# Kernel tuning notes

Measured on AMD Instinct MI355X. Metric: run time of the kernel, lower is better.

## Reference

```python
import jax, jax.numpy as jnp
import numpy as np

N_NODES = 100000
IN_DIM = 128
HID = 128
N_EDGES = 1600000
N_PAIRS = 500000


def setup_inputs() -> dict:
    key = jax.random.key(0)
    ks = jax.random.split(key, 16)

    def lin(k, fan_out, fan_in):
        s = 1.0 / np.sqrt(fan_in)
        kw, kb = jax.random.split(k)
        W = jax.random.uniform(kw, (fan_out, fan_in), jnp.float32, -s, s)
        b = jax.random.uniform(kb, (fan_out,), jnp.float32, -s, s)
        return W, b

    x = jax.random.normal(ks[0], (N_NODES, IN_DIM), jnp.float32)
    edge_index = jax.random.randint(ks[1], (2, N_EDGES), 0, N_NODES, jnp.int64)
    edge_pairs = jax.random.randint(ks[2], (N_PAIRS, 2), 0, N_NODES, jnp.int64)

    # SAGEConv 1: lin_l (neighbor aggr, with bias), lin_r (root, no bias)
    W1l, b1l = lin(ks[3], HID, IN_DIM)
    W1r, _ = lin(ks[4], HID, IN_DIM)
    # SAGEConv 2
    W2l, b2l = lin(ks[5], HID, HID)
    W2r, _ = lin(ks[6], HID, HID)
    # MLP decoder
    Wm1, bm1 = lin(ks[7], HID, HID)
    Wm2, bm2 = lin(ks[8], HID // 2, HID)
    Wm3, bm3 = lin(ks[9], 1, HID // 2)

    return dict(x=x, edge_index=edge_index, edge_pairs=edge_pairs,
                W1l=W1l, b1l=b1l, W1r=W1r,
                W2l=W2l, b2l=b2l, W2r=W2r,
                Wm1=Wm1, bm1=bm1, Wm2=Wm2, bm2=bm2, Wm3=Wm3, bm3=bm3)


def _sage_conv(x, src, dst, Wl, bl, Wr):
    # mean aggregation of source-node features into destination nodes
    msg_sum = jax.ops.segment_sum(x[src], dst, num_segments=N_NODES)  # [N, D]
    cnt = jax.ops.segment_sum(jnp.ones((src.shape[0],), x.dtype), dst,
                              num_segments=N_NODES)
    aggr = msg_sum / jnp.maximum(cnt, 1.0)[:, None]
    return aggr @ Wl.T + bl + x @ Wr.T


def reference(x, edge_index, edge_pairs,
              W1l, b1l, W1r, W2l, b2l, W2r,
              Wm1, bm1, Wm2, bm2, Wm3, bm3):
    src, dst = edge_index[0], edge_index[1]
    # encode (eval mode: dropout = identity)
    h = jax.nn.relu(_sage_conv(x, src, dst, W1l, b1l, W1r))
    z = _sage_conv(h, src, dst, W2l, b2l, W2r)  # [N, HID]
    # decode
    hp = z[edge_pairs[:, 0]] * z[edge_pairs[:, 1]]  # [P, HID]
    hp = jax.nn.relu(hp @ Wm1.T + bm1)
    hp = jax.nn.relu(hp @ Wm2.T + bm2)
    return (hp @ Wm3.T + bm3).squeeze(-1)  # [P]
```

## Files before the change

kernel.cpp:

```cpp
#include <hip/hip_runtime.h>
#include <stdint.h>

typedef _Float16 half8 __attribute__((ext_vector_type(8)));
typedef float float4v __attribute__((ext_vector_type(4)));

constexpr int kN = 100000;
constexpr int kE = 1600000;
constexpr int kP = 500000;
constexpr int NBS = (kN + 255) / 256;
constexpr int CT2 = kN / 32;
constexpr int DT2 = kP / 32;

__global__ void deg_kernel(const int* __restrict__ dst, int* __restrict__ deg) {
    int e = blockIdx.x * blockDim.x + threadIdx.x;
    if (e < kE) atomicAdd(&deg[dst[e]], 1);
}

__global__ void scan_block_sums(const int* __restrict__ deg, int* __restrict__ bsum) {
    __shared__ int red[256];
    int t = threadIdx.x;
    int i = blockIdx.x * 256 + t;
    red[t] = (i < kN) ? deg[i] : 0;
    __syncthreads();
    for (int s = 128; s > 0; s >>= 1) {
        if (t < s) red[t] += red[t + s];
        __syncthreads();
    }
    if (t == 0) bsum[blockIdx.x] = red[0];
}

__global__ void scan_bsums(const int* __restrict__ bsum, int* __restrict__ boff) {
    __shared__ int sm[512];
    int t = threadIdx.x;
    int orig = (t < NBS) ? bsum[t] : 0;
    sm[t] = orig;
    __syncthreads();
    for (int d = 1; d < 512; d <<= 1) {
        int u = (t >= d) ? sm[t - d] : 0;
        __syncthreads();
        sm[t] += u;
        __syncthreads();
    }
    if (t < NBS) boff[t] = sm[t] - orig;
}

__global__ void scan_write(const int* __restrict__ deg, const int* __restrict__ boff,
                           int* __restrict__ row_start, int* __restrict__ cursor) {
    __shared__ int sm[256];
    int t = threadIdx.x;
    int i = blockIdx.x * 256 + t;
    int v = (i < kN) ? deg[i] : 0;
    sm[t] = v;
    __syncthreads();
    for (int d = 1; d < 256; d <<= 1) {
        int u = (t >= d) ? sm[t - d] : 0;
        __syncthreads();
        sm[t] += u;
        __syncthreads();
    }
    int excl = sm[t] - v + boff[blockIdx.x];
    if (i < kN) { row_start[i] = excl; cursor[i] = excl; }
    if (i == kN - 1) row_start[kN] = excl + v;
}

__global__ void fill_kernel(const int* __restrict__ src, const int* __restrict__ dst,
                            int* __restrict__ cursor, int* __restrict__ srcs) {
    int e = blockIdx.x * blockDim.x + threadIdx.x;
    if (e < kE) {
        int p = atomicAdd(&cursor[dst[e]], 1);
        srcs[p] = src[e];
    }
}

__global__ void cvt_x_kernel(const float* __restrict__ x, _Float16* __restrict__ xh) {
    const int i = (blockIdx.x * 256 + threadIdx.x) * 8;
    if (i >= kN * 128) return;
    const float4 a = *(const float4*)&x[i];
    const float4 b = *(const float4*)&x[i + 4];
    half8 v;
    v[0] = (_Float16)a.x; v[1] = (_Float16)a.y; v[2] = (_Float16)a.z; v[3] = (_Float16)a.w;
    v[4] = (_Float16)b.x; v[5] = (_Float16)b.y; v[6] = (_Float16)b.z; v[7] = (_Float16)b.w;
    *(half8*)&xh[i] = v;
}

__global__ void cvt_w_kernel(
    const float* __restrict__ W1l, const float* __restrict__ W1r,
    const float* __restrict__ W2l, const float* __restrict__ W2r,
    const float* __restrict__ Wm1, const float* __restrict__ Wm2,
    _Float16* __restrict__ CW1h, _Float16* __restrict__ CW1e,
    _Float16* __restrict__ CW2h, _Float16* __restrict__ CW2e,
    _Float16* __restrict__ M1h,  _Float16* __restrict__ M2h)
{
    const int i = blockIdx.x * 256 + threadIdx.x;
    if (i < 32768) {
        const int o = i >> 8, k = i & 255;
        const float w = (k < 128) ? W1l[o * 128 + k] : W1r[o * 128 + k - 128];
        const _Float16 h = (_Float16)w;
        CW1h[i] = h; CW1e[i] = (_Float16)(w - (float)h);
    } else if (i < 65536) {
        const int j = i - 32768;
        const int o = j >> 8, k = j & 255;
        const float w = (k < 128) ? W2l[o * 128 + k] : W2r[o * 128 + k - 128];
        const _Float16 h = (_Float16)w;
        CW2h[j] = h; CW2e[j] = (_Float16)(w - (float)h);
    } else if (i < 81920) {
        const int j = i - 65536;
        M1h[j] = (_Float16)Wm1[j];
    } else if (i < 90112) {
        const int j = i - 81920;
        M2h[j] = (_Float16)Wm2[j];
    }
}

template <bool RELU>
__global__ __launch_bounds__(256, 3) void conv_mfma(
    const _Float16* __restrict__ xin,
    const int* __restrict__ row_start,
    const int* __restrict__ srcs,
    const _Float16* __restrict__ Wh,
    const _Float16* __restrict__ We,
    const float* __restrict__ bias,
    _Float16* __restrict__ out)
{
    __shared__ __align__(16) _Float16 stg_all[4 * 32 * 136];
    const int wInB = threadIdx.x >> 6;
    _Float16* stg  = &stg_all[wInB * (32 * 136)];
    const int l = threadIdx.x & 63;
    const int p = l & 15;
    const int q = l >> 4;
    const int tile = blockIdx.x * 4 + wInB;
    if (tile >= CT2) return;
    const int c = p * 8;
    const int lbase = l & 48;

    for (int sub = 0; sub < 8; sub++) {
        const int n  = tile * 32 + sub * 4 + q;
        const int j0 = row_start[n], j1 = row_start[n + 1];
        const int cnt = j1 - j0;
        float facc[8];
#pragma unroll
        for (int u = 0; u < 8; u++) facc[u] = 0.f;

        for (int jc = j0; jc < j1; jc += 16) {
            const int m = j1 - jc;
            const int myidx = (jc + p < j1) ? srcs[jc + p] : 0;
            half8 rows[16];
#pragma unroll
            for (int i = 0; i < 16; i++) {
                const int s = __shfl(myidx, lbase + i);
                rows[i] = *(const half8*)&xin[(size_t)s * 128 + c];
            }
#pragma unroll
            for (int i = 0; i < 16; i++) {
                if (i < m) {
#pragma unroll
                    for (int u = 0; u < 8; u++) facc[u] += (float)rows[i][u];
                }
            }
        }
        const float inv = 1.0f / (float)(cnt > 1 ? cnt : 1);
        half8 hv;
#pragma unroll
        for (int u = 0; u < 8; u++) hv[u] = (_Float16)(facc[u] * inv);
        *(half8*)&stg[(sub * 4 + q) * 136 + c] = hv;
    }

    half8 rt[2][4];
#pragma unroll
    for (int m = 0; m < 2; m++)
#pragma unroll
        for (int kt = 0; kt < 4; kt++)
            rt[m][kt] = *(const half8*)&xin[(size_t)(tile * 32 + m * 16 + p) * 128 + kt * 32 + q * 8];

    half8 amf[2][4];
#pragma unroll
    for (int m = 0; m < 2; m++)
#pragma unroll
        for (int kt = 0; kt < 4; kt++)
            amf[m][kt] = *(const half8*)&stg[(m * 16 + p) * 136 + kt * 32 + q * 8];

    float4v acc[2][8];
#pragma unroll
    for (int nt = 0; nt < 8; nt++) {
        const float b = bias[nt * 16 + p];
#pragma unroll
        for (int m = 0; m < 2; m++) {
            acc[m][nt][0] = b; acc[m][nt][1] = b; acc[m][nt][2] = b; acc[m][nt][3] = b;
        }
    }
#pragma unroll
    for (int kt = 0; kt < 8; kt++) {
        const half8 a0 = (kt < 4) ? amf[0][kt] : rt[0][kt - 4];
        const half8 a1 = (kt < 4) ? amf[1][kt] : rt[1][kt - 4];
#pragma unroll
        for (int nt = 0; nt < 8; nt++) {
            const int widx = (nt * 16 + p) * 256 + kt * 32 + q * 8;
            const half8 bh = *(const half8*)&Wh[widx];
            const half8 be = *(const half8*)&We[widx];
            acc[0][nt] = __builtin_amdgcn_mfma_f32_16x16x32_f16(a0, bh, acc[0][nt], 0, 0, 0);
            acc[0][nt] = __builtin_amdgcn_mfma_f32_16x16x32_f16(a0, be, acc[0][nt], 0, 0, 0);
            acc[1][nt] = __builtin_amdgcn_mfma_f32_16x16x32_f16(a1, bh, acc[1][nt], 0, 0, 0);
            acc[1][nt] = __builtin_amdgcn_mfma_f32_16x16x32_f16(a1, be, acc[1][nt], 0, 0, 0);
        }
    }

#pragma unroll
    for (int m = 0; m < 2; m++)
#pragma unroll
        for (int nt = 0; nt < 8; nt++)
#pragma unroll
            for (int r = 0; r < 4; r++) {
                float v = acc[m][nt][r];
                if (RELU) v = fmaxf(v, 0.f);
                stg[(m * 16 + q * 4 + r) * 136 + nt * 16 + p] = (_Float16)v;
            }
#pragma unroll
    for (int it = 0; it < 8; it++) {
        const int row = it * 4 + q;
        *(half8*)&out[(size_t)(tile * 32 + row) * 128 + c] =
            *(const half8*)&stg[row * 136 + c];
    }
}

__global__ __launch_bounds__(256, 3) void decoder_mfma(
    const _Float16* __restrict__ z,
    const int* __restrict__ pairs,
    const _Float16* __restrict__ M1h, const float* __restrict__ bm1,
    const _Float16* __restrict__ M2h, const float* __restrict__ bm2,
    const float* __restrict__ Wm3, const float* __restrict__ bm3,
    float* __restrict__ outv)
{
    __shared__ __align__(16) _Float16 buf_all[4 * 32 * 136];
    const int wInB = threadIdx.x >> 6;
    _Float16* buf  = &buf_all[wInB * (32 * 136)];
    const int l = threadIdx.x & 63;
    const int p = l & 15;
    const int q = l >> 4;
    const int tile = blockIdx.x * 4 + wInB;
    if (tile >= DT2) return;
    const int c = p * 8;

    int2 ab[8];
#pragma unroll
    for (int it = 0; it < 8; it++)
        ab[it] = *(const int2*)&pairs[(size_t)(tile * 32 + it * 4 + q) * 2];
    half8 za[8], zb[8];
#pragma unroll
    for (int it = 0; it < 8; it++) {
        za[it] = *(const half8*)&z[(size_t)ab[it].x * 128 + c];
        zb[it] = *(const half8*)&z[(size_t)ab[it].y * 128 + c];
    }
#pragma unroll
    for (int it = 0; it < 8; it++)
        *(half8*)&buf[(it * 4 + q) * 136 + c] = za[it] * zb[it];

    half8 a1[2][4];
#pragma unroll
    for (int m = 0; m < 2; m++)
#pragma unroll
        for (int kt = 0; kt < 4; kt++)
            a1[m][kt] = *(const half8*)&buf[(m * 16 + p) * 136 + kt * 32 + q * 8];

    float4v acc1[2][8];
#pragma unroll
    for (int nt = 0; nt < 8; nt++) {
        const float b = bm1[nt * 16 + p];
#pragma unroll
        for (int m = 0; m < 2; m++) {
            acc1[m][nt][0] = b; acc1[m][nt][1] = b; acc1[m][nt][2] = b; acc1[m][nt][3] = b;
        }
    }
#pragma unroll
    for (int kt = 0; kt < 4; kt++)
#pragma unroll
        for (int nt = 0; nt < 8; nt++) {
            const half8 bh = *(const half8*)&M1h[(nt * 16 + p) * 128 + kt * 32 + q * 8];
            acc1[0][nt] = __builtin_amdgcn_mfma_f32_16x16x32_f16(a1[0][kt], bh, acc1[0][nt], 0, 0, 0);
            acc1[1][nt] = __builtin_amdgcn_mfma_f32_16x16x32_f16(a1[1][kt], bh, acc1[1][nt], 0, 0, 0);
        }

#pragma unroll
    for (int m = 0; m < 2; m++)
#pragma unroll
        for (int nt = 0; nt < 8; nt++)
#pragma unroll
            for (int r = 0; r < 4; r++)
                buf[(m * 16 + q * 4 + r) * 136 + nt * 16 + p] =
                    (_Float16)fmaxf(acc1[m][nt][r], 0.f);

    half8 a2[2][4];
#pragma unroll
    for (int m = 0; m < 2; m++)
#pragma unroll
        for (int kt = 0; kt < 4; kt++)
            a2[m][kt] = *(const half8*)&buf[(m * 16 + p) * 136 + kt * 32 + q * 8];

    float4v acc2[2][4];
#pragma unroll
    for (int nt = 0; nt < 4; nt++) {
        const float b = bm2[nt * 16 + p];
#pragma unroll
        for (int m = 0; m < 2; m++) {
            acc2[m][nt][0] = b; acc2[m][nt][1] = b; acc2[m][nt][2] = b; acc2[m][nt][3] = b;
        }
    }
#pragma unroll
    for (int kt = 0; kt < 4; kt++)
#pragma unroll
        for (int nt = 0; nt < 4; nt++) {
            const half8 bh = *(const half8*)&M2h[(nt * 16 + p) * 128 + kt * 32 + q * 8];
            acc2[0][nt] = __builtin_amdgcn_mfma_f32_16x16x32_f16(a2[0][kt], bh, acc2[0][nt], 0, 0, 0);
            acc2[1][nt] = __builtin_amdgcn_mfma_f32_16x16x32_f16(a2[1][kt], bh, acc2[1][nt], 0, 0, 0);
        }

    float wm3v[4];
#pragma unroll
    for (int nt = 0; nt < 4; nt++) wm3v[nt] = Wm3[nt * 16 + p];
    const float b3 = bm3[0];
#pragma unroll
    for (int m = 0; m < 2; m++) {
        float part[4];
#pragma unroll
        for (int r = 0; r < 4; r++) part[r] = 0.f;
#pragma unroll
        for (int nt = 0; nt < 4; nt++)
#pragma unroll
            for (int r = 0; r < 4; r++)
                part[r] += fmaxf(acc2[m][nt][r], 0.f) * wm3v[nt];
#pragma unroll
        for (int s = 1; s <= 8; s <<= 1)
#pragma unroll
            for (int r = 0; r < 4; r++) part[r] += __shfl_xor(part[r], s);
        if (p == 0) {
            float4 o = make_float4(part[0] + b3, part[1] + b3, part[2] + b3, part[3] + b3);
            *(float4*)&outv[tile * 32 + m * 16 + q * 4] = o;
        }
    }
}

extern "C" void kernel_launch(void* const* d_in, const int* in_sizes, int n_in,
                              void* d_out, int out_size, void* d_ws, size_t ws_size,
                              hipStream_t stream) {
    const float* x   = (const float*)d_in[0];
    const int*   src = (const int*)d_in[1];
    const int*   dst = src + kE;
    const int*   ep  = (const int*)d_in[2];
    const float* W1l = (const float*)d_in[3];
    const float* b1l = (const float*)d_in[4];
    const float* W1r = (const float*)d_in[5];
    const float* W2l = (const float*)d_in[6];
    const float* b2l = (const float*)d_in[7];
    const float* W2r = (const float*)d_in[8];
    const float* Wm1 = (const float*)d_in[9];
    const float* bm1 = (const float*)d_in[10];
    const float* Wm2 = (const float*)d_in[11];
    const float* bm2 = (const float*)d_in[12];
    const float* Wm3 = (const float*)d_in[13];
    const float* bm3 = (const float*)d_in[14];
    float* outv = (float*)d_out;

    char* ws = (char*)d_ws;
    size_t off = 0;
    auto alloc = [&](size_t bytes) -> void* {
        void* p = ws + off;
        off += bytes;
        off = (off + 255) & ~(size_t)255;
        return p;
    };
    int*      deg       = (int*)alloc((size_t)kN * 4);
    int*      row_start = (int*)alloc((size_t)(kN + 1) * 4);
    int*      cursor    = (int*)alloc((size_t)kN * 4);
    int*      bsum      = (int*)alloc(512 * 4);
    int*      boff      = (int*)alloc(512 * 4);
    int*      srcs      = (int*)alloc((size_t)kE * 4);
    _Float16* xh        = (_Float16*)alloc((size_t)kN * 128 * 2);
    _Float16* hh        = (_Float16*)alloc((size_t)kN * 128 * 2);
    _Float16* zh        = (_Float16*)alloc((size_t)kN * 128 * 2);
    _Float16* CW1h      = (_Float16*)alloc(128 * 256 * 2);
    _Float16* CW1e      = (_Float16*)alloc(128 * 256 * 2);
    _Float16* CW2h      = (_Float16*)alloc(128 * 256 * 2);
    _Float16* CW2e      = (_Float16*)alloc(128 * 256 * 2);
    _Float16* M1h       = (_Float16*)alloc(128 * 128 * 2);
    _Float16* M2h       = (_Float16*)alloc(64 * 128 * 2);

    hipMemsetAsync(deg, 0, (size_t)kN * sizeof(int), stream);
    deg_kernel<<<(kE + 255) / 256, 256, 0, stream>>>(dst, deg);
    scan_block_sums<<<NBS, 256, 0, stream>>>(deg, bsum);
    scan_bsums<<<1, 512, 0, stream>>>(bsum, boff);
    scan_write<<<NBS, 256, 0, stream>>>(deg, boff, row_start, cursor);
    fill_kernel<<<(kE + 255) / 256, 256, 0, stream>>>(src, dst, cursor, srcs);

    cvt_x_kernel<<<(kN * 128 / 8 + 255) / 256, 256, 0, stream>>>(x, xh);
    cvt_w_kernel<<<352, 256, 0, stream>>>(W1l, W1r, W2l, W2r, Wm1, Wm2,
                                          CW1h, CW1e, CW2h, CW2e, M1h, M2h);

    const int convBlocks = (CT2 + 3) / 4;
    conv_mfma<true><<<convBlocks, 256, 0, stream>>>(xh, row_start, srcs, CW1h, CW1e, b1l, hh);
    conv_mfma<false><<<convBlocks, 256, 0, stream>>>(hh, row_start, srcs, CW2h, CW2e, b2l, zh);

    const int decBlocks = (DT2 + 3) / 4;
    decoder_mfma<<<decBlocks, 256, 0, stream>>>(
        zh, ep, M1h, bm1, M2h, bm2, Wm3, bm3, outv);
}
```

Before: 686.0 us.

## Software-pipeline neighbor gathers in conv and persistent prefetching decoder

The conv kernel now handles 16-node tiles per wave instead of 32 and raises the occupancy hint. Neighbor-row gathers are double-buffered across four sub-rows, with the first 24 neighbors loaded in 8-row batches and the remainder in a tail loop. The decoder becomes a persistent grid-stride kernel with a fixed grid, prefetching the next tile's pair indices and z rows while the current tile's MLP runs on MFMA. Both changes aim to hide gather latency, at the cost of more register pressure and more complex control flow; the srcs buffer is padded so the speculative index reads stay in bounds.

```diff
diff --git a/kernel.cpp b/kernel.cpp
--- a/kernel.cpp
+++ b/kernel.cpp
@@ -8,7 +8,7 @@
 constexpr int kE = 1600000;
 constexpr int kP = 500000;
 constexpr int NBS = (kN + 255) / 256;
-constexpr int CT2 = kN / 32;
+constexpr int CT3 = kN / 16;
 constexpr int DT2 = kP / 32;
 
 __global__ void deg_kernel(const int* __restrict__ dst, int* __restrict__ deg) {
@@ -113,7 +113,7 @@
 }
 
 template <bool RELU>
-__global__ __launch_bounds__(256, 3) void conv_mfma(
+__global__ __launch_bounds__(256, 4) void conv_mfma(
     const _Float16* __restrict__ xin,
     const int* __restrict__ row_start,
     const int* __restrict__ srcs,
@@ -122,103 +122,159 @@
     const float* __restrict__ bias,
     _Float16* __restrict__ out)
 {
-    __shared__ __align__(16) _Float16 stg_all[4 * 32 * 136];
+    __shared__ __align__(16) _Float16 stg_all[4 * 16 * 136];
     const int wInB = threadIdx.x >> 6;
-    _Float16* stg  = &stg_all[wInB * (32 * 136)];
+    _Float16* stg  = &stg_all[wInB * (16 * 136)];
     const int l = threadIdx.x & 63;
     const int p = l & 15;
     const int q = l >> 4;
     const int tile = blockIdx.x * 4 + wInB;
-    if (tile >= CT2) return;
+    if (tile >= CT3) return;
     const int c = p * 8;
     const int lbase = l & 48;
 
-    for (int sub = 0; sub < 8; sub++) {
-        const int n  = tile * 32 + sub * 4 + q;
-        const int j0 = row_start[n], j1 = row_start[n + 1];
-        const int cnt = j1 - j0;
-        float facc[8];
-#pragma unroll
-        for (int u = 0; u < 8; u++) facc[u] = 0.f;
-
-        for (int jc = j0; jc < j1; jc += 16) {
-            const int m = j1 - jc;
-            const int myidx = (jc + p < j1) ? srcs[jc + p] : 0;
-            half8 rows[16];
-#pragma unroll
-            for (int i = 0; i < 16; i++) {
-                const int s = __shfl(myidx, lbase + i);
-                rows[i] = *(const half8*)&xin[(size_t)s * 128 + c];
-            }
-#pragma unroll
-            for (int i = 0; i < 16; i++) {
-                if (i < m) {
-#pragma unroll
-                    for (int u = 0; u < 8; u++) facc[u] += (float)rows[i][u];
-                }
-            }
-        }
-        const float inv = 1.0f / (float)(cnt > 1 ? cnt : 1);
-        half8 hv;
-#pragma unroll
-        for (int u = 0; u < 8; u++) hv[u] = (_Float16)(facc[u] * inv);
-        *(half8*)&stg[(sub * 4 + q) * 136 + c] = hv;
-    }
-
-    half8 rt[2][4];
-#pragma unroll
-    for (int m = 0; m < 2; m++)
-#pragma unroll
-        for (int kt = 0; kt < 4; kt++)
-            rt[m][kt] = *(const half8*)&xin[(size_t)(tile * 32 + m * 16 + p) * 128 + kt * 32 + q * 8];
-
-    half8 amf[2][4];
-#pragma unroll
-    for (int m = 0; m < 2; m++)
-#pragma unroll
-        for (int kt = 0; kt < 4; kt++)
-            amf[m][kt] = *(const half8*)&stg[(m * 16 + p) * 136 + kt * 32 + q * 8];
-
-    float4v acc[2][8];
+    int j0[4], j1[4], cnt[4];
+#pragma unroll
+    for (int s = 0; s < 4; s++) {
+        const int n = tile * 16 + s * 4 + q;
+        j0[s] = row_start[n];
+        j1[s] = row_start[n + 1];
+        cnt[s] = j1[s] - j0[s];
+    }
+    int idxA[4], idxB[4];
+#pragma unroll
+    for (int s = 0; s < 4; s++) {
+        const int tA = j0[s] + p;
+        const int vA = srcs[tA];
+        idxA[s] = (tA < j1[s]) ? vA : 0;
+        const int tB = j0[s] + 16 + (p & 7);
+        const int vB = srcs[tB];
+        idxB[s] = (tB < j1[s]) ? vB : 0;
+    }
+
+    float fa[8], fb[8];
+    half8 bufA[8], bufB[8];
+
+#define CONV_ISSUE(K, BUF)                                                   \
+    {                                                                        \
+        constexpr int s_ = (K) / 3, h_ = (K) % 3;                            \
+        const int src16 = (h_ < 2) ? idxA[s_] : idxB[s_];                    \
+        _Pragma("unroll")                                                    \
+        for (int i = 0; i < 8; i++) {                                        \
+            const int sidx = __shfl(src16, lbase + ((h_ == 1) ? 8 : 0) + i); \
+            BUF[i] = *(const half8*)&xin[(size_t)sidx * 128 + c];            \
+        }                                                                    \
+    }
+
+#define CONV_CONSUME(K, BUF)                                                 \
+    {                                                                        \
+        constexpr int s_ = (K) / 3, h_ = (K) % 3;                            \
+        float* fc = ((s_ & 1) ? fb : fa);                                    \
+        if (h_ == 0) {                                                       \
+            _Pragma("unroll")                                                \
+            for (int u = 0; u < 8; u++) fc[u] = 0.f;                         \
+        }                                                                    \
+        _Pragma("unroll")                                                    \
+        for (int i = 0; i < 8; i++) {                                        \
+            if (h_ * 8 + i < cnt[s_]) {                                      \
+                _Pragma("unroll")                                            \
+                for (int u = 0; u < 8; u++) fc[u] += (float)BUF[i][u];       \
+            }                                                                \
+        }                                                                    \
+    }
+
+#define CONV_FIN(S)                                                          \
+    {                                                                        \
+        float* fc = (((S) & 1) ? fb : fa);                                   \
+        int jc = j0[S] + 24;                                                 \
+        while (jc < j1[S]) {                                                 \
+            const int t4 = jc + (p & 3);                                     \
+            const int vi = srcs[t4];                                         \
+            const int myi = (t4 < j1[S]) ? vi : 0;                           \
+            half8 rbuf[4];                                                   \
+            _Pragma("unroll")                                                \
+            for (int i = 0; i < 4; i++) {                                    \
+                const int sidx = __shfl(myi, lbase + i);                     \
+                rbuf[i] = *(const half8*)&xin[(size_t)sidx * 128 + c];       \
+            }                                                                \
+            _Pragma("unroll")                                                \
+            for (int i = 0; i < 4; i++)                                      \
+                if (jc + i < j1[S]) {                                        \
+                    _Pragma("unroll")                                        \
+                    for (int u = 0; u < 8; u++) fc[u] += (float)rbuf[i][u];  \
+                }                                                            \
+            jc += 4;                                                         \
+        }                                                                    \
+        const float inv = 1.0f / (float)(cnt[S] > 1 ? cnt[S] : 1);           \
+        half8 hv;                                                            \
+        _Pragma("unroll")                                                    \
+        for (int u = 0; u < 8; u++) hv[u] = (_Float16)(fc[u] * inv);         \
+        *(half8*)&stg[((S) * 4 + q) * 136 + c] = hv;                         \
+    }
+
+    CONV_ISSUE(0, bufA);
+    CONV_ISSUE(1, bufB);
+    CONV_CONSUME(0, bufA);  CONV_ISSUE(2, bufA);
+    CONV_CONSUME(1, bufB);  CONV_ISSUE(3, bufB);
+    CONV_CONSUME(2, bufA);  CONV_FIN(0);  CONV_ISSUE(4, bufA);
+    CONV_CONSUME(3, bufB);  CONV_ISSUE(5, bufB);
+    CONV_CONSUME(4, bufA);  CONV_ISSUE(6, bufA);
+    CONV_CONSUME(5, bufB);  CONV_FIN(1);  CONV_ISSUE(7, bufB);
+    CONV_CONSUME(6, bufA);  CONV_ISSUE(8, bufA);
+    CONV_CONSUME(7, bufB);  CONV_ISSUE(9, bufB);
+    CONV_CONSUME(8, bufA);  CONV_FIN(2);  CONV_ISSUE(10, bufA);
+    CONV_CONSUME(9, bufB);  CONV_ISSUE(11, bufB);
+    CONV_CONSUME(10, bufA);
+    CONV_CONSUME(11, bufB); CONV_FIN(3);
+
+#undef CONV_ISSUE
+#undef CONV_CONSUME
+#undef CONV_FIN
+
+    half8 rt[4];
+#pragma unroll
+    for (int kt = 0; kt < 4; kt++)
+        rt[kt] = *(const half8*)&xin[(size_t)(tile * 16 + p) * 128 + kt * 32 + q * 8];
+
+    half8 am[4];
+#pragma unroll
+    for (int kt = 0; kt < 4; kt++)
+        am[kt] = *(const half8*)&stg[p * 136 + kt * 32 + q * 8];
+
+    float4v acc[8];
 #pragma unroll
     for (int nt = 0; nt < 8; nt++) {
         const float b = bias[nt * 16 + p];
-#pragma unroll
-        for (int m = 0; m < 2; m++) {
-            acc[m][nt][0] = b; acc[m][nt][1] = b; acc[m][nt][2] = b; acc[m][nt][3] = b;
-        }
+        acc[nt][0] = b; acc[nt][1] = b; acc[nt][2] = b; acc[nt][3] = b;
     }
 #pragma unroll
     for (int kt = 0; kt < 8; kt++) {
-        const half8 a0 = (kt < 4) ? amf[0][kt] : rt[0][kt - 4];
-        const half8 a1 = (kt < 4) ? amf[1][kt] : rt[1][kt - 4];
+        const half8 a = (kt < 4) ? am[kt] : rt[kt - 4];
 #pragma unroll
         for (int nt = 0; nt < 8; nt++) {
             const int widx = (nt * 16 + p) * 256 + kt * 32 + q * 8;
             const half8 bh = *(const half8*)&Wh[widx];
             const half8 be = *(const half8*)&We[widx];
-            acc[0][nt] = __builtin_amdgcn_mfma_f32_16x16x32_f16(a0, bh, acc[0][nt], 0, 0, 0);
-            acc[0][nt] = __builtin_amdgcn_mfma_f32_16x16x32_f16(a0, be, acc[0][nt], 0, 0, 0);
-            acc[1][nt] = __builtin_amdgcn_mfma_f32_16x16x32_f16(a1, bh, acc[1][nt], 0, 0, 0);
-            acc[1][nt] = __builtin_amdgcn_mfma_f32_16x16x32_f16(a1, be, acc[1][nt], 0, 0, 0);
-        }
-    }
-
-#pragma unroll
-    for (int m = 0; m < 2; m++)
-#pragma unroll
-        for (int nt = 0; nt < 8; nt++)
-#pragma unroll
-            for (int r = 0; r < 4; r++) {
-                float v = acc[m][nt][r];
-                if (RELU) v = fmaxf(v, 0.f);
-                stg[(m * 16 + q * 4 + r) * 136 + nt * 16 + p] = (_Float16)v;
-            }
-#pragma unroll
-    for (int it = 0; it < 8; it++) {
-        const int row = it * 4 + q;
-        *(half8*)&out[(size_t)(tile * 32 + row) * 128 + c] =
-            *(const half8*)&stg[row * 136 + c];
+            acc[nt] = __builtin_amdgcn_mfma_f32_16x16x32_f16(a, bh, acc[nt], 0, 0, 0);
+            acc[nt] = __builtin_amdgcn_mfma_f32_16x16x32_f16(a, be, acc[nt], 0, 0, 0);
+        }
+    }
+
+#pragma unroll
+    for (int nt = 0; nt < 8; nt++)
+#pragma unroll
+        for (int r = 0; r < 4; r++) {
+            float v = acc[nt][r];
+            if (RELU) v = fmaxf(v, 0.f);
+            stg[(q * 4 + r) * 136 + nt * 16 + p] = (_Float16)v;
+        }
+    {
+        const int row = l >> 2;
+        const int c2  = (l & 3) * 8;
+#pragma unroll
+        for (int i = 0; i < 4; i++)
+            *(half8*)&out[(size_t)(tile * 16 + row) * 128 + i * 32 + c2] =
+                *(const half8*)&stg[row * 136 + i * 32 + c2];
     }
 }
 
@@ -236,104 +292,136 @@
     const int l = threadIdx.x & 63;
     const int p = l & 15;
     const int q = l >> 4;
-    const int tile = blockIdx.x * 4 + wInB;
-    if (tile >= DT2) return;
+    const int wid = blockIdx.x * 4 + wInB;
+    const int nw  = gridDim.x * 4;
+    if (wid >= DT2) return;
     const int c = p * 8;
 
-    int2 ab[8];
-#pragma unroll
-    for (int it = 0; it < 8; it++)
-        ab[it] = *(const int2*)&pairs[(size_t)(tile * 32 + it * 4 + q) * 2];
+    const float b3 = bm3[0];
+    float wm3v[4];
+#pragma unroll
+    for (int nt = 0; nt < 4; nt++) wm3v[nt] = Wm3[nt * 16 + p];
+
+    int2 abCur[8], abNext[8];
+    {
+        const int tA = wid;
+        const int tB = (wid + nw < DT2) ? (wid + nw) : (DT2 - 1);
+#pragma unroll
+        for (int it = 0; it < 8; it++)
+            abCur[it] = *(const int2*)&pairs[(size_t)(tA * 32 + it * 4 + q) * 2];
+#pragma unroll
+        for (int it = 0; it < 8; it++)
+            abNext[it] = *(const int2*)&pairs[(size_t)(tB * 32 + it * 4 + q) * 2];
+    }
     half8 za[8], zb[8];
 #pragma unroll
     for (int it = 0; it < 8; it++) {
-        za[it] = *(const half8*)&z[(size_t)ab[it].x * 128 + c];
-        zb[it] = *(const half8*)&z[(size_t)ab[it].y * 128 + c];
-    }
-#pragma unroll
-    for (int it = 0; it < 8; it++)
-        *(half8*)&buf[(it * 4 + q) * 136 + c] = za[it] * zb[it];
-
-    half8 a1[2][4];
-#pragma unroll
-    for (int m = 0; m < 2; m++)
+        za[it] = *(const half8*)&z[(size_t)abCur[it].x * 128 + c];
+        zb[it] = *(const half8*)&z[(size_t)abCur[it].y * 128 + c];
+    }
+
+    for (int t = wid; t < DT2; t += nw) {
+        {
+            const int t2 = (t + 2 * nw < DT2) ? (t + 2 * nw) : (DT2 - 1);
+#pragma unroll
+            for (int it = 0; it < 8; it++)
+                abCur[it] = *(const int2*)&pairs[(size_t)(t2 * 32 + it * 4 + q) * 2];
+        }
+
+#pragma unroll
+        for (int it = 0; it < 8; it++)
+            *(half8*)&buf[(it * 4 + q) * 136 + c] = za[it] * zb[it];
+
+        const bool more = (t + nw < DT2);
+        if (more) {
+#pragma unroll
+            for (int it = 0; it < 8; it++) {
+                za[it] = *(const half8*)&z[(size_t)abNext[it].x * 128 + c];
+                zb[it] = *(const half8*)&z[(size_t)abNext[it].y * 128 + c];
+            }
+        }
+#pragma unroll
+        for (int it = 0; it < 8; it++) abNext[it] = abCur[it];
+
+        half8 a1[2][4];
+#pragma unroll
+        for (int m = 0; m < 2; m++)
+#pragma unroll
+            for (int kt = 0; kt < 4; kt++)
+                a1[m][kt] = *(const half8*)&buf[(m * 16 + p) * 136 + kt * 32 + q * 8];
+
+        float4v acc1[2][8];
+#pragma unroll
+        for (int nt = 0; nt < 8; nt++) {
+            const float b = bm1[nt * 16 + p];
+#pragma unroll
+            for (int m = 0; m < 2; m++) {
+                acc1[m][nt][0] = b; acc1[m][nt][1] = b;
+                acc1[m][nt][2] = b; acc1[m][nt][3] = b;
+            }
+        }
 #pragma unroll
         for (int kt = 0; kt < 4; kt++)
-            a1[m][kt] = *(const half8*)&buf[(m * 16 + p) * 136 + kt * 32 + q * 8];
-
-    float4v acc1[2][8];
-#pragma unroll
-    for (int nt = 0; nt < 8; nt++) {
-        const float b = bm1[nt * 16 + p];
+#pragma unroll
+            for (int nt = 0; nt < 8; nt++) {
+                const half8 bh = *(const half8*)&M1h[(nt * 16 + p) * 128 + kt * 32 + q * 8];
+                acc1[0][nt] = __builtin_amdgcn_mfma_f32_16x16x32_f16(a1[0][kt], bh, acc1[0][nt], 0, 0, 0);
+                acc1[1][nt] = __builtin_amdgcn_mfma_f32_16x16x32_f16(a1[1][kt], bh, acc1[1][nt], 0, 0, 0);
+            }
+
+#pragma unroll
+        for (int m = 0; m < 2; m++)
+#pragma unroll
+            for (int nt = 0; nt < 8; nt++)
+#pragma unroll
+                for (int r = 0; r < 4; r++)
+                    buf[(m * 16 + q * 4 + r) * 136 + nt * 16 + p] =
+                        (_Float16)fmaxf(acc1[m][nt][r], 0.f);
+
+        half8 a2[2][4];
+#pragma unroll
+        for (int m = 0; m < 2; m++)
+#pragma unroll
+            for (int kt = 0; kt < 4; kt++)
+                a2[m][kt] = *(const half8*)&buf[(m * 16 + p) * 136 + kt * 32 + q * 8];
+
+        float4v acc2[2][4];
+#pragma unroll
+        for (int nt = 0; nt < 4; nt++) {
+            const float b = bm2[nt * 16 + p];
+#pragma unroll
+            for (int m = 0; m < 2; m++) {
+                acc2[m][nt][0] = b; acc2[m][nt][1] = b;
+                acc2[m][nt][2] = b; acc2[m][nt][3] = b;
+            }
+        }
+#pragma unroll
+        for (int kt = 0; kt < 4; kt++)
+#pragma unroll
+            for (int nt = 0; nt < 4; nt++) {
+                const half8 bh = *(const half8*)&M2h[(nt * 16 + p) * 128 + kt * 32 + q * 8];
+                acc2[0][nt] = __builtin_amdgcn_mfma_f32_16x16x32_f16(a2[0][kt], bh, acc2[0][nt], 0, 0, 0);
+                acc2[1][nt] = __builtin_amdgcn_mfma_f32_16x16x32_f16(a2[1][kt], bh, acc2[1][nt], 0, 0, 0);
+            }
+
 #pragma unroll
         for (int m = 0; m < 2; m++) {
-            acc1[m][nt][0] = b; acc1[m][nt][1] = b; acc1[m][nt][2] = b; acc1[m][nt][3] = b;
-        }
-    }
-#pragma unroll
-    for (int kt = 0; kt < 4; kt++)
-#pragma unroll
-        for (int nt = 0; nt < 8; nt++) {
-            const half8 bh = *(const half8*)&M1h[(nt * 16 + p) * 128 + kt * 32 + q * 8];
-            acc1[0][nt] = __builtin_amdgcn_mfma_f32_16x16x32_f16(a1[0][kt], bh, acc1[0][nt], 0, 0, 0);
-            acc1[1][nt] = __builtin_amdgcn_mfma_f32_16x16x32_f16(a1[1][kt], bh, acc1[1][nt], 0, 0, 0);
-        }
-
-#pragma unroll
-    for (int m = 0; m < 2; m++)
-#pragma unroll
-        for (int nt = 0; nt < 8; nt++)
-#pragma unroll
-            for (int r = 0; r < 4; r++)
-                buf[(m * 16 + q * 4 + r) * 136 + nt * 16 + p] =
-                    (_Float16)fmaxf(acc1[m][nt][r], 0.f);
-
-    half8 a2[2][4];
-#pragma unroll
-    for (int m = 0; m < 2; m++)
-#pragma unroll
-        for (int kt = 0; kt < 4; kt++)
-            a2[m][kt] = *(const half8*)&buf[(m * 16 + p) * 136 + kt * 32 + q * 8];
-
-    float4v acc2[2][4];
-#pragma unroll
-    for (int nt = 0; nt < 4; nt++) {
-        const float b = bm2[nt * 16 + p];
-#pragma unroll
-        for (int m = 0; m < 2; m++) {
-            acc2[m][nt][0] = b; acc2[m][nt][1] = b; acc2[m][nt][2] = b; acc2[m][nt][3] = b;
-        }
-    }
-#pragma unroll
-    for (int kt = 0; kt < 4; kt++)
-#pragma unroll
-        for (int nt = 0; nt < 4; nt++) {
-            const half8 bh = *(const half8*)&M2h[(nt * 16 + p) * 128 + kt * 32 + q * 8];
-            acc2[0][nt] = __builtin_amdgcn_mfma_f32_16x16x32_f16(a2[0][kt], bh, acc2[0][nt], 0, 0, 0);
-            acc2[1][nt] = __builtin_amdgcn_mfma_f32_16x16x32_f16(a2[1][kt], bh, acc2[1][nt], 0, 0, 0);
-        }
-
-    float wm3v[4];
-#pragma unroll
-    for (int nt = 0; nt < 4; nt++) wm3v[nt] = Wm3[nt * 16 + p];
-    const float b3 = bm3[0];
-#pragma unroll
-    for (int m = 0; m < 2; m++) {
-        float part[4];
-#pragma unroll
-        for (int r = 0; r < 4; r++) part[r] = 0.f;
-#pragma unroll
-        for (int nt = 0; nt < 4; nt++)
-#pragma unroll
-            for (int r = 0; r < 4; r++)
-                part[r] += fmaxf(acc2[m][nt][r], 0.f) * wm3v[nt];
-#pragma unroll
-        for (int s = 1; s <= 8; s <<= 1)
-#pragma unroll
-            for (int r = 0; r < 4; r++) part[r] += __shfl_xor(part[r], s);
-        if (p == 0) {
-            float4 o = make_float4(part[0] + b3, part[1] + b3, part[2] + b3, part[3] + b3);
-            *(float4*)&outv[tile * 32 + m * 16 + q * 4] = o;
+            float part[4];
+#pragma unroll
+            for (int r = 0; r < 4; r++) part[r] = 0.f;
+#pragma unroll
+            for (int nt = 0; nt < 4; nt++)
+#pragma unroll
+                for (int r = 0; r < 4; r++)
+                    part[r] += fmaxf(acc2[m][nt][r], 0.f) * wm3v[nt];
+#pragma unroll
+            for (int s = 1; s <= 8; s <<= 1)
+#pragma unroll
+                for (int r = 0; r < 4; r++) part[r] += __shfl_xor(part[r], s);
+            if (p == 0) {
+                float4 o = make_float4(part[0] + b3, part[1] + b3, part[2] + b3, part[3] + b3);
+                *(float4*)&outv[t * 32 + m * 16 + q * 4] = o;
+            }
         }
     }
 }
@@ -372,7 +460,7 @@
     int*      cursor    = (int*)alloc((size_t)kN * 4);
     int*      bsum      = (int*)alloc(512 * 4);
     int*      boff      = (int*)alloc(512 * 4);
-    int*      srcs      = (int*)alloc((size_t)kE * 4);
+    int*      srcs      = (int*)alloc((size_t)(kE + 64) * 4);
     _Float16* xh        = (_Float16*)alloc((size_t)kN * 128 * 2);
     _Float16* hh        = (_Float16*)alloc((size_t)kN * 128 * 2);
     _Float16* zh        = (_Float16*)alloc((size_t)kN * 128 * 2);
@@ -394,11 +482,10 @@
     cvt_w_kernel<<<352, 256, 0, stream>>>(W1l, W1r, W2l, W2r, Wm1, Wm2,
                                           CW1h, CW1e, CW2h, CW2e, M1h, M2h);
 
-    const int convBlocks = (CT2 + 3) / 4;
+    const int convBlocks = (CT3 + 3) / 4;
     conv_mfma<true><<<convBlocks, 256, 0, stream>>>(xh, row_start, srcs, CW1h, CW1e, b1l, hh);
     conv_mfma<false><<<convBlocks, 256, 0, stream>>>(hh, row_start, srcs, CW2h, CW2e, b2l, zh);
 
-    const int decBlocks = (DT2 + 3) / 4;
-    decoder_mfma<<<decBlocks, 256, 0, stream>>>(
+    decoder_mfma<<<768, 256, 0, stream>>>(
         zh, ep, M1h, bm1, M2h, bm2, Wm3, bm3, outv);
 }
```

Measured after the change: 960.8 us. +40.0%, slower.

## Halve conv tile to 16 rows, prefetch neighbor indices, drop second atomic pass

Applied to the files above, without the earlier changes.

The CSR build now records each edge's slot from the degree atomic, so the fill pass becomes a plain scatter with no second round of atomics. The conv kernel moves from 32-node to 16-node tiles per wave, with smaller LDS and accumulator state and a higher occupancy hint, to get more waves in flight for the gather. Neighbor index lists are loaded up front for all four sub-rows and gathered in 8-row chunks, which suits the average degree of about 16. The price is fewer rows per weight-fragment load in the MFMA stage and an extra slot array of edge length.

```diff
diff --git a/kernel.cpp b/kernel.cpp
--- a/kernel.cpp
+++ b/kernel.cpp
@@ -8,12 +8,13 @@
 constexpr int kE = 1600000;
 constexpr int kP = 500000;
 constexpr int NBS = (kN + 255) / 256;
-constexpr int CT2 = kN / 32;
+constexpr int CT3 = kN / 16;
 constexpr int DT2 = kP / 32;
 
-__global__ void deg_kernel(const int* __restrict__ dst, int* __restrict__ deg) {
+__global__ void deg_slot_kernel(const int* __restrict__ dst,
+                                int* __restrict__ deg, int* __restrict__ slot) {
     int e = blockIdx.x * blockDim.x + threadIdx.x;
-    if (e < kE) atomicAdd(&deg[dst[e]], 1);
+    if (e < kE) slot[e] = atomicAdd(&deg[dst[e]], 1);
 }
 
 __global__ void scan_block_sums(const int* __restrict__ deg, int* __restrict__ bsum) {
@@ -45,7 +46,7 @@
 }
 
 __global__ void scan_write(const int* __restrict__ deg, const int* __restrict__ boff,
-                           int* __restrict__ row_start, int* __restrict__ cursor) {
+                           int* __restrict__ row_start) {
     __shared__ int sm[256];
     int t = threadIdx.x;
     int i = blockIdx.x * 256 + t;
@@ -59,17 +60,15 @@
         __syncthreads();
     }
     int excl = sm[t] - v + boff[blockIdx.x];
-    if (i < kN) { row_start[i] = excl; cursor[i] = excl; }
+    if (i < kN) row_start[i] = excl;
     if (i == kN - 1) row_start[kN] = excl + v;
 }
 
-__global__ void fill_kernel(const int* __restrict__ src, const int* __restrict__ dst,
-                            int* __restrict__ cursor, int* __restrict__ srcs) {
+__global__ void fill2_kernel(const int* __restrict__ src, const int* __restrict__ dst,
+                             const int* __restrict__ row_start,
+                             const int* __restrict__ slot, int* __restrict__ srcs) {
     int e = blockIdx.x * blockDim.x + threadIdx.x;
-    if (e < kE) {
-        int p = atomicAdd(&cursor[dst[e]], 1);
-        srcs[p] = src[e];
-    }
+    if (e < kE) srcs[row_start[dst[e]] + slot[e]] = src[e];
 }
 
 __global__ void cvt_x_kernel(const float* __restrict__ x, _Float16* __restrict__ xh) {
@@ -113,7 +112,7 @@
 }
 
 template <bool RELU>
-__global__ __launch_bounds__(256, 3) void conv_mfma(
+__global__ __launch_bounds__(256, 4) void conv_mfma(
     const _Float16* __restrict__ xin,
     const int* __restrict__ row_start,
     const int* __restrict__ srcs,
@@ -122,37 +121,58 @@
     const float* __restrict__ bias,
     _Float16* __restrict__ out)
 {
-    __shared__ __align__(16) _Float16 stg_all[4 * 32 * 136];
+    __shared__ __align__(16) _Float16 stg_all[4 * 16 * 136];
     const int wInB = threadIdx.x >> 6;
-    _Float16* stg  = &stg_all[wInB * (32 * 136)];
+    _Float16* stg  = &stg_all[wInB * (16 * 136)];
     const int l = threadIdx.x & 63;
     const int p = l & 15;
     const int q = l >> 4;
     const int tile = blockIdx.x * 4 + wInB;
-    if (tile >= CT2) return;
+    if (tile >= CT3) return;
     const int c = p * 8;
     const int lbase = l & 48;
 
-    for (int sub = 0; sub < 8; sub++) {
-        const int n  = tile * 32 + sub * 4 + q;
-        const int j0 = row_start[n], j1 = row_start[n + 1];
-        const int cnt = j1 - j0;
+    int j0[4], j1[4];
+#pragma unroll
+    for (int s = 0; s < 4; s++) {
+        const int n = tile * 16 + s * 4 + q;
+        j0[s] = row_start[n];
+        j1[s] = row_start[n + 1];
+    }
+    int idx16[4];
+#pragma unroll
+    for (int s = 0; s < 4; s++) {
+        const int tA = j0[s] + p;
+        const int v  = srcs[tA];
+        idx16[s] = (tA < j1[s]) ? v : 0;
+    }
+
+    for (int s = 0; s < 4; s++) {
+        const int cnt = j1[s] - j0[s];
         float facc[8];
 #pragma unroll
         for (int u = 0; u < 8; u++) facc[u] = 0.f;
-
-        for (int jc = j0; jc < j1; jc += 16) {
-            const int m = j1 - jc;
-            const int myidx = (jc + p < j1) ? srcs[jc + p] : 0;
-            half8 rows[16];
-#pragma unroll
-            for (int i = 0; i < 16; i++) {
-                const int s = __shfl(myidx, lbase + i);
-                rows[i] = *(const half8*)&xin[(size_t)s * 128 + c];
+        int h = 0;
+        for (int jc = j0[s]; jc < j1[s]; jc += 8, h++) {
+            int myidx;
+            if (h < 2) {
+                myidx = idx16[s];
+            } else {
+                const int tB = jc + (p & 7);
+                const int v  = srcs[tB];
+                myidx = (tB < j1[s]) ? v : 0;
             }
-#pragma unroll
-            for (int i = 0; i < 16; i++) {
-                if (i < m) {
+            const int lsh = lbase + ((h == 1) ? 8 : 0);
+            half8 rows[8];
+#pragma unroll
+            for (int i = 0; i < 8; i++) {
+                const int sidx = __shfl(myidx, lsh + i);
+                rows[i] = *(const half8*)&xin[(size_t)sidx * 128 + c];
+            }
+            const int rem = j1[s] - jc;
+#pragma unroll
+            for (int i = 0; i < 8; i++) {
+                if (i < rem) {
 #pragma unroll
                     for (int u = 0; u < 8; u++) facc[u] += (float)rows[i][u];
                 }
@@ -162,63 +182,53 @@
         half8 hv;
 #pragma unroll
         for (int u = 0; u < 8; u++) hv[u] = (_Float16)(facc[u] * inv);
-        *(half8*)&stg[(sub * 4 + q) * 136 + c] = hv;
-    }
-
-    half8 rt[2][4];
-#pragma unroll
-    for (int m = 0; m < 2; m++)
-#pragma unroll
-        for (int kt = 0; kt < 4; kt++)
-            rt[m][kt] = *(const half8*)&xin[(size_t)(tile * 32 + m * 16 + p) * 128 + kt * 32 + q * 8];
-
-    half8 amf[2][4];
-#pragma unroll
-    for (int m = 0; m < 2; m++)
-#pragma unroll
-        for (int kt = 0; kt < 4; kt++)
-            amf[m][kt] = *(const half8*)&stg[(m * 16 + p) * 136 + kt * 32 + q * 8];
-
-    float4v acc[2][8];
+        *(half8*)&stg[(s * 4 + q) * 136 + c] = hv;
+    }
+
+    half8 rt[4];
+#pragma unroll
+    for (int kt = 0; kt < 4; kt++)
+        rt[kt] = *(const half8*)&xin[(size_t)(tile * 16 + p) * 128 + kt * 32 + q * 8];
+
+    half8 am[4];
+#pragma unroll
+    for (int kt = 0; kt < 4; kt++)
+        am[kt] = *(const half8*)&stg[p * 136 + kt * 32 + q * 8];
+
+    float4v acc[8];
 #pragma unroll
     for (int nt = 0; nt < 8; nt++) {
         const float b = bias[nt * 16 + p];
-#pragma unroll
-        for (int m = 0; m < 2; m++) {
-            acc[m][nt][0] = b; acc[m][nt][1] = b; acc[m][nt][2] = b; acc[m][nt][3] = b;
-        }
+        acc[nt][0] = b; acc[nt][1] = b; acc[nt][2] = b; acc[nt][3] = b;
     }
 #pragma unroll
     for (int kt = 0; kt < 8; kt++) {
-        const half8 a0 = (kt < 4) ? amf[0][kt] : rt[0][kt - 4];
-        const half8 a1 = (kt < 4) ? amf[1][kt] : rt[1][kt - 4];
+        const half8 a = (kt < 4) ? am[kt] : rt[kt - 4];
 #pragma unroll
         for (int nt = 0; nt < 8; nt++) {
             const int widx = (nt * 16 + p) * 256 + kt * 32 + q * 8;
             const half8 bh = *(const half8*)&Wh[widx];
             const half8 be = *(const half8*)&We[widx];
-            acc[0][nt] = __builtin_amdgcn_mfma_f32_16x16x32_f16(a0, bh, acc[0][nt], 0, 0, 0);
-            acc[0][nt] = __builtin_amdgcn_mfma_f32_16x16x32_f16(a0, be, acc[0][nt], 0, 0, 0);
-            acc[1][nt] = __builtin_amdgcn_mfma_f32_16x16x32_f16(a1, bh, acc[1][nt], 0, 0, 0);
-            acc[1][nt] = __builtin_amdgcn_mfma_f32_16x16x32_f16(a1, be, acc[1][nt], 0, 0, 0);
-        }
-    }
-
-#pragma unroll
-    for (int m = 0; m < 2; m++)
-#pragma unroll
-        for (int nt = 0; nt < 8; nt++)
-#pragma unroll
-            for (int r = 0; r < 4; r++) {
-                float v = acc[m][nt][r];
-                if (RELU) v = fmaxf(v, 0.f);
-                stg[(m * 16 + q * 4 + r) * 136 + nt * 16 + p] = (_Float16)v;
-            }
-#pragma unroll
-    for (int it = 0; it < 8; it++) {
-        const int row = it * 4 + q;
-        *(half8*)&out[(size_t)(tile * 32 + row) * 128 + c] =
-            *(const half8*)&stg[row * 136 + c];
+            acc[nt] = __builtin_amdgcn_mfma_f32_16x16x32_f16(a, bh, acc[nt], 0, 0, 0);
+            acc[nt] = __builtin_amdgcn_mfma_f32_16x16x32_f16(a, be, acc[nt], 0, 0, 0);
+        }
+    }
+
+#pragma unroll
+    for (int nt = 0; nt < 8; nt++)
+#pragma unroll
+        for (int r = 0; r < 4; r++) {
+            float v = acc[nt][r];
+            if (RELU) v = fmaxf(v, 0.f);
+            stg[(q * 4 + r) * 136 + nt * 16 + p] = (_Float16)v;
+        }
+    {
+        const int row = l >> 2;
+        const int c2  = (l & 3) * 8;
+#pragma unroll
+        for (int i = 0; i < 4; i++)
+            *(half8*)&out[(size_t)(tile * 16 + row) * 128 + i * 32 + c2] =
+                *(const half8*)&stg[row * 136 + i * 32 + c2];
     }
 }
 
@@ -369,10 +379,10 @@
     };
     int*      deg       = (int*)alloc((size_t)kN * 4);
     int*      row_start = (int*)alloc((size_t)(kN + 1) * 4);
-    int*      cursor    = (int*)alloc((size_t)kN * 4);
+    int*      slot      = (int*)alloc((size_t)kE * 4);
     int*      bsum      = (int*)alloc(512 * 4);
     int*      boff      = (int*)alloc(512 * 4);
-    int*      srcs      = (int*)alloc((size_t)kE * 4);
+    int*      srcs      = (int*)alloc((size_t)(kE + 64) * 4);
     _Float16* xh        = (_Float16*)alloc((size_t)kN * 128 * 2);
     _Float16* hh        = (_Float16*)alloc((size_t)kN * 128 * 2);
     _Float16* zh        = (_Float16*)alloc((size_t)kN * 128 * 2);
@@ -384,17 +394,17 @@
     _Float16* M2h       = (_Float16*)alloc(64 * 128 * 2);
 
     hipMemsetAsync(deg, 0, (size_t)kN * sizeof(int), stream);
-    deg_kernel<<<(kE + 255) / 256, 256, 0, stream>>>(dst, deg);
+    deg_slot_kernel<<<(kE + 255) / 256, 256, 0, stream>>>(dst, deg, slot);
     scan_block_sums<<<NBS, 256, 0, stream>>>(deg, bsum);
     scan_bsums<<<1, 512, 0, stream>>>(bsum, boff);
-    scan_write<<<NBS, 256, 0, stream>>>(deg, boff, row_start, cursor);
-    fill_kernel<<<(kE + 255) / 256, 256, 0, stream>>>(src, dst, cursor, srcs);
+    scan_write<<<NBS, 256, 0, stream>>>(deg, boff, row_start);
+    fill2_kernel<<<(kE + 255) / 256, 256, 0, stream>>>(src, dst, row_start, slot, srcs);
 
     cvt_x_kernel<<<(kN * 128 / 8 + 255) / 256, 256, 0, stream>>>(x, xh);
     cvt_w_kernel<<<352, 256, 0, stream>>>(W1l, W1r, W2l, W2r, Wm1, Wm2,
                                           CW1h, CW1e, CW2h, CW2e, M1h, M2h);
 
-    const int convBlocks = (CT2 + 3) / 4;
+    const int convBlocks = (CT3 + 3) / 4;
     conv_mfma<true><<<convBlocks, 256, 0, stream>>>(xh, row_start, srcs, CW1h, CW1e, b1l, hh);
     conv_mfma<false><<<convBlocks, 256, 0, stream>>>(hh, row_start, srcs, CW2h, CW2e, b2l, zh);
 
```

Result: faster. 615.7 us (-10.3%).
